# Kernel tuning notes

Hardware: AMD Instinct MI355X
Metric: run time of the kernel (lower is better)

The kernel has to match this reference:

```python
import jax, jax.numpy as jnp
import numpy as np

NUM_ITERATIONS = 5
EPSILON_0 = 1.0
EPS = 1e-20


def setup_inputs() -> dict:
    key = jax.random.key(0)
    k1, k2 = jax.random.split(key)
    B, NIN, NOUT = 8192, 3072, 512
    x = jax.random.uniform(k1, (B, NIN), dtype=jnp.float32)
    w = jax.random.uniform(k2, (NOUT, NIN), dtype=jnp.float32)
    # weights setter normalizes rows to sum to 1
    w = w / w.sum(axis=1, keepdims=True)
    h_initial = jnp.full((NOUT,), 1.0 / NOUT, dtype=jnp.float32)
    return {"x": x, "weights": w, "h_initial": h_initial}


def reference(x, weights, h_initial):
    # x: [B, NIN], weights: [NOUT, NIN], h_initial: [NOUT]
    x = x / (x.sum(axis=1, keepdims=True) + EPS)  # input normalization in forward()
    B = x.shape[0]
    h = jnp.broadcast_to(h_initial[None, :], (B, h_initial.shape[0]))

    def step(h, _):
        # Original: h_w = h[:,:,None]*W[None]; h_w /= h_w.sum(1,keepdim)+eps;
        #           h_w = (h_w * x[:,None,:]).sum(-1)
        # Equivalent without materializing [B, NOUT, NIN]:
        denom = h @ weights                       # [B, NIN] = sum_n h_bn W_nk
        h_w = h * ((x / (denom + EPS)) @ weights.T)  # [B, NOUT]
        h_new = h + EPSILON_0 * h_w               # epsilon_0 > 0 branch
        h_new = h_new / (h_new.sum(axis=1, keepdims=True) + EPS)
        return h_new, None

    h, _ = jax.lax.scan(step, h, None, length=NUM_ITERATIONS)
    return h
```

## Files before the change

kernel.cpp:

```cpp
#include <hip/hip_runtime.h>


#define NIN 3072
#define NOUT 512

using f32x4 = __attribute__((ext_vector_type(4))) float;
using i32x8 = __attribute__((ext_vector_type(8))) int;

union frag32 { i32x8 v; uint4 q[2]; };

#define MFMA128(A, B, C) \
    __builtin_amdgcn_mfma_scale_f32_16x16x128_f8f6f4( \
        (A), (B), (C), 0, 0, 0, (int)0x7f7f7f7f, 0, (int)0x7f7f7f7f)
#define MFMA128_F6(A, B, C) \
    __builtin_amdgcn_mfma_scale_f32_16x16x128_f8f6f4( \
        (A), (B), (C), 0, 2, 0, (int)0x7f7f7f7f, 0, (int)0x7f7f7f7f)

__device__ __forceinline__ unsigned short f2bf(float f) {
    unsigned int u = __builtin_bit_cast(unsigned int, f);
    return (unsigned short)((u + 0x7fffu + ((u >> 16) & 1u)) >> 16);
}
__device__ __forceinline__ float bf2f(unsigned short s) {
    unsigned int u = ((unsigned int)s) << 16;
    return __builtin_bit_cast(float, u);
}

__device__ __forceinline__ unsigned enc_fp6(float p) {
    if (p < 1.9375f) {
        int q = (int)rintf(p * 8.0f);
        return (unsigned)q;
    }
    if (p < 3.875f) {
        int m = (int)rintf((p - 2.0f) * 4.0f);
        return (m > 7) ? 24u : (16u + (unsigned)m);
    }
    int m = (int)rintf((p - 4.0f) * 2.0f);
    if (m > 7) m = 7;
    return 24u + (unsigned)m;
}

__device__ __forceinline__ void load6(frag32& f, const unsigned char* p) {
    const uint2* q = reinterpret_cast<const uint2*>(p);
    uint2 a = q[0], b = q[1], c = q[2];
    f.v = (i32x8){(int)a.x, (int)a.y, (int)b.x, (int)b.y, (int)c.x, (int)c.y, 0, 0};
}

#define LDS_BARRIER() do {                                   \
    asm volatile("s_waitcnt lgkmcnt(0)" ::: "memory");       \
    __builtin_amdgcn_s_barrier();                            \
    asm volatile("" ::: "memory");                           \
} while (0)

__global__ void prep_all(const float* __restrict__ x,
                         const float* __restrict__ W,
                         const float* __restrict__ h_init,
                         unsigned short* __restrict__ X2,
                         unsigned char* __restrict__ W1,
                         unsigned char* __restrict__ W2,
                         float* __restrict__ d0part) {
    __shared__ float tile[64][132];
    __shared__ float wsum[4];
    const int bb = blockIdx.x;
    const int t  = threadIdx.x;

    if (bb < 192) {
        const int s  = bb >> 3, nc = bb & 7;
        const int n0 = nc * 64, k0 = s * 128;

        {
            int r8 = t >> 5, c4 = (t & 31) << 2;
            #pragma unroll
            for (int pass = 0; pass < 8; ++pass) {
                int r = pass * 8 + r8;
                float4 v = *reinterpret_cast<const float4*>(
                    &W[(size_t)(n0 + r) * NIN + k0 + c4]);
                tile[r][c4] = v.x; tile[r][c4 + 1] = v.y;
                tile[r][c4 + 2] = v.z; tile[r][c4 + 3] = v.w;
            }
        }
        __syncthreads();

        {
            int ntl = t >> 6, l = t & 63, lo = l & 15, hi = l >> 4;
            int n_loc = ntl * 16 + lo;
            int kk = hi * 32;
            unsigned int words[8];
            #pragma unroll
            for (int q = 0; q < 8; ++q) {
                float v0 = tile[n_loc][kk + q * 4 + 0] * 4096.0f;
                float v1 = tile[n_loc][kk + q * 4 + 1] * 4096.0f;
                float v2 = tile[n_loc][kk + q * 4 + 2] * 4096.0f;
                float v3 = tile[n_loc][kk + q * 4 + 3] * 4096.0f;
                int pk = __builtin_amdgcn_cvt_pk_fp8_f32(v0, v1, 0, false);
                pk     = __builtin_amdgcn_cvt_pk_fp8_f32(v2, v3, pk, true);
                words[q] = (unsigned int)pk;
            }
            uint4* dst = reinterpret_cast<uint4*>(
                W2 + ((size_t)((s * 32 + nc * 4 + ntl) * 64 + l)) * 32);
            dst[0] = *reinterpret_cast<uint4*>(&words[0]);
            dst[1] = *reinterpret_cast<uint4*>(&words[4]);
        }

        {
            int w8 = t >> 5, r5 = t & 31, l15 = r5 & 15, hs = r5 >> 4;
            int hi = ((nc & 1) << 1) + hs;
            int l  = hi * 16 + l15;
            int c  = nc >> 1;
            int kout_loc = w8 * 16 + l15;
            unsigned int dw[6] = {0, 0, 0, 0, 0, 0};
            #pragma unroll
            for (int j = 0; j < 32; ++j) {
                float p = tile[hs * 32 + j][kout_loc] * 8192.0f;
                unsigned c6 = enc_fp6(p);
                int bit = 6 * j, di = bit >> 5, off = bit & 31;
                dw[di] |= c6 << off;
                if (off > 26) dw[di + 1] |= c6 >> (32 - off);
            }
            uint2* d2 = reinterpret_cast<uint2*>(
                W1 + ((size_t)(((s * 8 + w8) * 4 + c) * 64 + l)) * 24);
            d2[0] = make_uint2(dw[0], dw[1]);
            d2[1] = make_uint2(dw[2], dw[3]);
            d2[2] = make_uint2(dw[4], dw[5]);
        }

        if (t < 128) {
            float ssum = 0.f;
            #pragma unroll 8
            for (int r = 0; r < 64; ++r)
                ssum += h_init[n0 + r] * tile[r][t];
            d0part[(size_t)nc * NIN + k0 + t] = ssum;
        }
    } else {
        const int b = bb - 192;
        const float4* r4 = reinterpret_cast<const float4*>(x + (size_t)b * NIN);
        float s = 0.f;
        float4 v0 = r4[t], v1 = r4[t + 256], v2 = r4[t + 512];
        s = v0.x + v0.y + v0.z + v0.w + v1.x + v1.y + v1.z + v1.w + v2.x + v2.y + v2.z + v2.w;
        #pragma unroll
        for (int off = 32; off > 0; off >>= 1) s += __shfl_down(s, off, 64);
        int w = t >> 6, l = t & 63;
        if (l == 0) wsum[w] = s;
        __syncthreads();
        float inv = 16.0f / (wsum[0] + wsum[1] + wsum[2] + wsum[3] + 1e-20f);
        unsigned short* orow = X2 + (size_t)b * NIN;
        #pragma unroll
        for (int c = 0; c < 3; ++c) {
            float4 v = (c == 0) ? v0 : (c == 1) ? v1 : v2;
            ushort4 o;
            o.x = f2bf(v.x * inv); o.y = f2bf(v.y * inv);
            o.z = f2bf(v.z * inv); o.w = f2bf(v.w * inv);
            *reinterpret_cast<ushort4*>(orow + (t + c * 256) * 4) = o;
        }
    }
}

__global__ __launch_bounds__(512, 1) void nnmf_main(
    const unsigned short* __restrict__ X2,
    const unsigned char* __restrict__ W1,
    const unsigned char* __restrict__ W2,
    const float* __restrict__ d0part,
    const float* __restrict__ h_init,
    float* __restrict__ out)
{
    __shared__ unsigned char  h8_lds[32 * 528];
    __shared__ float          h32_lds[32 * 516];
    __shared__ unsigned short x_lds[32 * 136];
    __shared__ unsigned char  r8_lds[32 * 144];
    __shared__ float red[8][32];

    const int tid = threadIdx.x;
    const int w  = tid >> 6;
    const int l  = tid & 63;
    const int lo = l & 15;
    const int hi = l >> 4;
    const int b0 = blockIdx.x * 32;

    for (int idx = tid; idx < 32 * 512; idx += 512) {
        int r = idx >> 9, c = idx & 511;
        h32_lds[r * 516 + c] = h_init[c];
    }

    const int xrow = tid >> 4, xcc = tid & 15;
    const uint4* xg = reinterpret_cast<const uint4*>(X2 + (size_t)(b0 + xrow) * NIN + xcc * 8);
    unsigned short* xdst = &x_lds[xrow * 136 + xcc * 8];

    const unsigned char* w1base = W1 + ((size_t)(w * 4) * 64 + l) * 24;
    const unsigned char* w2base = W2 + (size_t)w * 8192 + (size_t)l * 32;

    *reinterpret_cast<uint4*>(xdst) = xg[0];
    uint4 xnext = xg[16];
    frag32 w1buf[4];
    __syncthreads();

    const float DSCL = 4.76837158203125e-07f;
    const float TS   = 1.0f / 65536.0f;
    f32x4 tacc[2][4];

    for (int it = 0; it < 5; ++it) {
        #pragma unroll
        for (int m = 0; m < 2; ++m)
            #pragma unroll
            for (int nt = 0; nt < 4; ++nt)
                tacc[m][nt] = (f32x4){0.f, 0.f, 0.f, 0.f};

        for (int s = 0; s < 24; ++s) {
            const int sn  = (s + 1 == 24) ? 0 : s + 1;
            const int sn2 = (s + 2 >= 24) ? (s + 2 - 24) : s + 2;

            frag32 w2v[4];
            {
                const unsigned char* w2p = w2base + (size_t)s * 65536;
                #pragma unroll
                for (int nt = 0; nt < 4; ++nt) {
                    const uint4* p = reinterpret_cast<const uint4*>(w2p + nt * 2048);
                    w2v[nt].q[0] = p[0];
                    w2v[nt].q[1] = p[1];
                }
            }

            f32x4 d0 = {0,0,0,0}, d1 = {0,0,0,0};
            float dv = 0.f;
            if (it == 0) {
                const float* dp = d0part + s * 128 + w * 16 + lo;
                float sm = 1e-20f;
                #pragma unroll
                for (int j = 0; j < 8; ++j) sm += dp[(size_t)j * NIN];
                dv = 1.0f / sm;
            } else {
                #pragma unroll
                for (int c = 0; c < 4; ++c) {
                    frag32 ha0, ha1;
                    const uint4* p0 = reinterpret_cast<const uint4*>(
                        &h8_lds[lo * 528 + c * 128 + hi * 32]);
                    const uint4* p1 = reinterpret_cast<const uint4*>(
                        &h8_lds[(16 + lo) * 528 + c * 128 + hi * 32]);
                    ha0.q[0] = p0[0]; ha0.q[1] = p0[1];
                    ha1.q[0] = p1[0]; ha1.q[1] = p1[1];
                    d0 = MFMA128_F6(ha0.v, w1buf[c].v, d0);
                    d1 = MFMA128_F6(ha1.v, w1buf[c].v, d1);
                }
            }

            #pragma unroll
            for (int i = 0; i < 4; ++i) {
                int row0 = hi * 4 + i;
                float x0 = bf2f(x_lds[row0 * 136 + w * 16 + lo]);
                float x1 = bf2f(x_lds[(16 + row0) * 136 + w * 16 + lo]);
                float r0, r1;
                if (it == 0) { r0 = x0 * dv; r1 = x1 * dv; }
                else {
                    r0 = x0 * __builtin_amdgcn_rcpf(fmaf(d0[i], DSCL, 1e-20f));
                    r1 = x1 * __builtin_amdgcn_rcpf(fmaf(d1[i], DSCL, 1e-20f));
                }
                int c0 = __builtin_amdgcn_cvt_pk_fp8_f32(r0, r0, 0, false);
                int c1 = __builtin_amdgcn_cvt_pk_fp8_f32(r1, r1, 0, false);
                r8_lds[row0 * 144 + w * 16 + lo] = (unsigned char)(c0 & 0xff);
                r8_lds[(16 + row0) * 144 + w * 16 + lo] = (unsigned char)(c1 & 0xff);
            }
            LDS_BARRIER();

            frag32 ra0, ra1;
            {
                const uint4* p0 = reinterpret_cast<const uint4*>(&r8_lds[lo * 144 + hi * 32]);
                const uint4* p1 = reinterpret_cast<const uint4*>(&r8_lds[(16 + lo) * 144 + hi * 32]);
                ra0.q[0] = p0[0]; ra0.q[1] = p0[1];
                ra1.q[0] = p1[0]; ra1.q[1] = p1[1];
            }
            #pragma unroll
            for (int nt = 0; nt < 2; ++nt) {
                tacc[0][nt] = MFMA128(ra0.v, w2v[nt].v, tacc[0][nt]);
                tacc[1][nt] = MFMA128(ra1.v, w2v[nt].v, tacc[1][nt]);
            }

            if (it > 0 || s == 23) {
                const unsigned char* w1p = w1base + (size_t)sn * 49152;
                #pragma unroll
                for (int c = 0; c < 4; ++c)
                    load6(w1buf[c], w1p + c * 1536);
            }

            #pragma unroll
            for (int nt = 2; nt < 4; ++nt) {
                tacc[0][nt] = MFMA128(ra0.v, w2v[nt].v, tacc[0][nt]);
                tacc[1][nt] = MFMA128(ra1.v, w2v[nt].v, tacc[1][nt]);
            }

            *reinterpret_cast<uint4*>(xdst) = xnext;
            xnext = xg[(size_t)sn2 * 16];
            LDS_BARRIER();
        }

        float hv_[2][4][4];
        float p[2][4];
        #pragma unroll
        for (int m = 0; m < 2; ++m)
            #pragma unroll
            for (int i = 0; i < 4; ++i) p[m][i] = 0.f;

        #pragma unroll
        for (int m = 0; m < 2; ++m)
            #pragma unroll
            for (int nt = 0; nt < 4; ++nt)
                #pragma unroll
                for (int i = 0; i < 4; ++i) {
                    int row = m * 16 + hi * 4 + i;
                    int col = w * 64 + nt * 16 + lo;
                    float hv = h32_lds[row * 516 + col];
                    float v = hv * (1.f + tacc[m][nt][i] * TS);
                    hv_[m][nt][i] = v;
                    p[m][i] += v;
                }
        #pragma unroll
        for (int mask = 1; mask < 16; mask <<= 1)
            #pragma unroll
            for (int m = 0; m < 2; ++m)
                #pragma unroll
                for (int i = 0; i < 4; ++i)
                    p[m][i] += __shfl_xor(p[m][i], mask, 64);
        if (lo == 0) {
            #pragma unroll
            for (int m = 0; m < 2; ++m)
                #pragma unroll
                for (int i = 0; i < 4; ++i)
                    red[w][m * 16 + hi * 4 + i] = p[m][i];
        }
        __syncthreads();
        float inv[2][4];
        #pragma unroll
        for (int m = 0; m < 2; ++m)
            #pragma unroll
            for (int i = 0; i < 4; ++i) {
                int row = m * 16 + hi * 4 + i;
                float S = 0.f;
                #pragma unroll
                for (int ww = 0; ww < 8; ++ww) S += red[ww][row];
                inv[m][i] = 1.f / (S + 1e-20f);
            }

        if (it < 4) {
            #pragma unroll
            for (int m = 0; m < 2; ++m)
                #pragma unroll
                for (int nt = 0; nt < 4; ++nt)
                    #pragma unroll
                    for (int i = 0; i < 4; ++i) {
                        int row = m * 16 + hi * 4 + i;
                        int col = w * 64 + nt * 16 + lo;
                        float hv = hv_[m][nt][i] * inv[m][i];
                        h32_lds[row * 516 + col] = hv;
                        int c = __builtin_amdgcn_cvt_pk_fp8_f32(hv * 256.0f, hv * 256.0f, 0, false);
                        h8_lds[row * 528 + col] = (unsigned char)(c & 0xff);
                    }
            __syncthreads();
        } else {
            #pragma unroll
            for (int m = 0; m < 2; ++m)
                #pragma unroll
                for (int nt = 0; nt < 4; ++nt)
                    #pragma unroll
                    for (int i = 0; i < 4; ++i) {
                        int row = m * 16 + hi * 4 + i;
                        int col = w * 64 + nt * 16 + lo;
                        out[(size_t)(b0 + row) * 512 + col] = hv_[m][nt][i] * inv[m][i];
                    }
        }
    }
}

extern "C" void kernel_launch(void* const* d_in, const int* in_sizes, int n_in,
                              void* d_out, int out_size, void* d_ws, size_t ws_size,
                              hipStream_t stream) {
    const float* x   = (const float*)d_in[0];
    const float* wgt = (const float*)d_in[1];
    const float* h0  = (const float*)d_in[2];
    float* out = (float*)d_out;

    unsigned short* X2 = (unsigned short*)d_ws;
    unsigned char*  W1 = (unsigned char*)((char*)d_ws + 50331648);
    unsigned char*  W2 = (unsigned char*)((char*)d_ws + 51511296);
    float* d0part      = (float*)((char*)d_ws + 53084160);

    prep_all<<<8384, 256, 0, stream>>>(x, wgt, h0, X2, W1, W2, d0part);
    nnmf_main<<<256, 512, 0, stream>>>(X2, W1, W2, d0part, h0, out);
}
```

Before: 388.0 us.

## Fuse input row normalization into main kernel, read raw fp32 x directly

Drops the separate pass that normalized x and wrote a bf16 copy to workspace. The main kernel now streams raw fp32 x, accumulates row sums during the first iteration, and folds the normalization factor into the h update. This removes one full read and write of the large input. The cost is twice the x bytes loaded per iteration and a larger LDS tile. The d0part layout is also transposed so it can be read with vector loads.

```diff
diff --git a/kernel.cpp b/kernel.cpp
--- a/kernel.cpp
+++ b/kernel.cpp
@@ -16,15 +16,6 @@
     __builtin_amdgcn_mfma_scale_f32_16x16x128_f8f6f4( \
         (A), (B), (C), 0, 2, 0, (int)0x7f7f7f7f, 0, (int)0x7f7f7f7f)
 
-__device__ __forceinline__ unsigned short f2bf(float f) {
-    unsigned int u = __builtin_bit_cast(unsigned int, f);
-    return (unsigned short)((u + 0x7fffu + ((u >> 16) & 1u)) >> 16);
-}
-__device__ __forceinline__ float bf2f(unsigned short s) {
-    unsigned int u = ((unsigned int)s) << 16;
-    return __builtin_bit_cast(float, u);
-}
-
 __device__ __forceinline__ unsigned enc_fp6(float p) {
     if (p < 1.9375f) {
         int q = (int)rintf(p * 8.0f);
@@ -51,111 +42,84 @@
     asm volatile("" ::: "memory");                           \
 } while (0)
 
-__global__ void prep_all(const float* __restrict__ x,
-                         const float* __restrict__ W,
-                         const float* __restrict__ h_init,
-                         unsigned short* __restrict__ X2,
-                         unsigned char* __restrict__ W1,
-                         unsigned char* __restrict__ W2,
-                         float* __restrict__ d0part) {
+__global__ void prep_w(const float* __restrict__ W,
+                       const float* __restrict__ h_init,
+                       unsigned char* __restrict__ W1,
+                       unsigned char* __restrict__ W2,
+                       float* __restrict__ d0part) {
     __shared__ float tile[64][132];
-    __shared__ float wsum[4];
     const int bb = blockIdx.x;
     const int t  = threadIdx.x;
-
-    if (bb < 192) {
-        const int s  = bb >> 3, nc = bb & 7;
-        const int n0 = nc * 64, k0 = s * 128;
-
-        {
-            int r8 = t >> 5, c4 = (t & 31) << 2;
-            #pragma unroll
-            for (int pass = 0; pass < 8; ++pass) {
-                int r = pass * 8 + r8;
-                float4 v = *reinterpret_cast<const float4*>(
-                    &W[(size_t)(n0 + r) * NIN + k0 + c4]);
-                tile[r][c4] = v.x; tile[r][c4 + 1] = v.y;
-                tile[r][c4 + 2] = v.z; tile[r][c4 + 3] = v.w;
-            }
-        }
-        __syncthreads();
-
-        {
-            int ntl = t >> 6, l = t & 63, lo = l & 15, hi = l >> 4;
-            int n_loc = ntl * 16 + lo;
-            int kk = hi * 32;
-            unsigned int words[8];
-            #pragma unroll
-            for (int q = 0; q < 8; ++q) {
-                float v0 = tile[n_loc][kk + q * 4 + 0] * 4096.0f;
-                float v1 = tile[n_loc][kk + q * 4 + 1] * 4096.0f;
-                float v2 = tile[n_loc][kk + q * 4 + 2] * 4096.0f;
-                float v3 = tile[n_loc][kk + q * 4 + 3] * 4096.0f;
-                int pk = __builtin_amdgcn_cvt_pk_fp8_f32(v0, v1, 0, false);
-                pk     = __builtin_amdgcn_cvt_pk_fp8_f32(v2, v3, pk, true);
-                words[q] = (unsigned int)pk;
-            }
-            uint4* dst = reinterpret_cast<uint4*>(
-                W2 + ((size_t)((s * 32 + nc * 4 + ntl) * 64 + l)) * 32);
-            dst[0] = *reinterpret_cast<uint4*>(&words[0]);
-            dst[1] = *reinterpret_cast<uint4*>(&words[4]);
-        }
-
-        {
-            int w8 = t >> 5, r5 = t & 31, l15 = r5 & 15, hs = r5 >> 4;
-            int hi = ((nc & 1) << 1) + hs;
-            int l  = hi * 16 + l15;
-            int c  = nc >> 1;
-            int kout_loc = w8 * 16 + l15;
-            unsigned int dw[6] = {0, 0, 0, 0, 0, 0};
-            #pragma unroll
-            for (int j = 0; j < 32; ++j) {
-                float p = tile[hs * 32 + j][kout_loc] * 8192.0f;
-                unsigned c6 = enc_fp6(p);
-                int bit = 6 * j, di = bit >> 5, off = bit & 31;
-                dw[di] |= c6 << off;
-                if (off > 26) dw[di + 1] |= c6 >> (32 - off);
-            }
-            uint2* d2 = reinterpret_cast<uint2*>(
-                W1 + ((size_t)(((s * 8 + w8) * 4 + c) * 64 + l)) * 24);
-            d2[0] = make_uint2(dw[0], dw[1]);
-            d2[1] = make_uint2(dw[2], dw[3]);
-            d2[2] = make_uint2(dw[4], dw[5]);
-        }
-
-        if (t < 128) {
-            float ssum = 0.f;
-            #pragma unroll 8
-            for (int r = 0; r < 64; ++r)
-                ssum += h_init[n0 + r] * tile[r][t];
-            d0part[(size_t)nc * NIN + k0 + t] = ssum;
-        }
-    } else {
-        const int b = bb - 192;
-        const float4* r4 = reinterpret_cast<const float4*>(x + (size_t)b * NIN);
-        float s = 0.f;
-        float4 v0 = r4[t], v1 = r4[t + 256], v2 = r4[t + 512];
-        s = v0.x + v0.y + v0.z + v0.w + v1.x + v1.y + v1.z + v1.w + v2.x + v2.y + v2.z + v2.w;
-        #pragma unroll
-        for (int off = 32; off > 0; off >>= 1) s += __shfl_down(s, off, 64);
-        int w = t >> 6, l = t & 63;
-        if (l == 0) wsum[w] = s;
-        __syncthreads();
-        float inv = 16.0f / (wsum[0] + wsum[1] + wsum[2] + wsum[3] + 1e-20f);
-        unsigned short* orow = X2 + (size_t)b * NIN;
-        #pragma unroll
-        for (int c = 0; c < 3; ++c) {
-            float4 v = (c == 0) ? v0 : (c == 1) ? v1 : v2;
-            ushort4 o;
-            o.x = f2bf(v.x * inv); o.y = f2bf(v.y * inv);
-            o.z = f2bf(v.z * inv); o.w = f2bf(v.w * inv);
-            *reinterpret_cast<ushort4*>(orow + (t + c * 256) * 4) = o;
-        }
+    const int s  = bb >> 3, nc = bb & 7;
+    const int n0 = nc * 64, k0 = s * 128;
+
+    {
+        int r8 = t >> 5, c4 = (t & 31) << 2;
+        #pragma unroll
+        for (int pass = 0; pass < 8; ++pass) {
+            int r = pass * 8 + r8;
+            float4 v = *reinterpret_cast<const float4*>(
+                &W[(size_t)(n0 + r) * NIN + k0 + c4]);
+            tile[r][c4] = v.x; tile[r][c4 + 1] = v.y;
+            tile[r][c4 + 2] = v.z; tile[r][c4 + 3] = v.w;
+        }
+    }
+    __syncthreads();
+
+    {
+        int ntl = t >> 6, l = t & 63, lo = l & 15, hi = l >> 4;
+        int n_loc = ntl * 16 + lo;
+        int kk = hi * 32;
+        unsigned int words[8];
+        #pragma unroll
+        for (int q = 0; q < 8; ++q) {
+            float v0 = tile[n_loc][kk + q * 4 + 0] * 4096.0f;
+            float v1 = tile[n_loc][kk + q * 4 + 1] * 4096.0f;
+            float v2 = tile[n_loc][kk + q * 4 + 2] * 4096.0f;
+            float v3 = tile[n_loc][kk + q * 4 + 3] * 4096.0f;
+            int pk = __builtin_amdgcn_cvt_pk_fp8_f32(v0, v1, 0, false);
+            pk     = __builtin_amdgcn_cvt_pk_fp8_f32(v2, v3, pk, true);
+            words[q] = (unsigned int)pk;
+        }
+        uint4* dst = reinterpret_cast<uint4*>(
+            W2 + ((size_t)((s * 32 + nc * 4 + ntl) * 64 + l)) * 32);
+        dst[0] = *reinterpret_cast<uint4*>(&words[0]);
+        dst[1] = *reinterpret_cast<uint4*>(&words[4]);
+    }
+
+    {
+        int w8 = t >> 5, r5 = t & 31, l15 = r5 & 15, hs = r5 >> 4;
+        int hi = ((nc & 1) << 1) + hs;
+        int l  = hi * 16 + l15;
+        int c  = nc >> 1;
+        int kout_loc = w8 * 16 + l15;
+        unsigned int dw[6] = {0, 0, 0, 0, 0, 0};
+        #pragma unroll
+        for (int j = 0; j < 32; ++j) {
+            float p = tile[hs * 32 + j][kout_loc] * 8192.0f;
+            unsigned c6 = enc_fp6(p);
+            int bit = 6 * j, di = bit >> 5, off = bit & 31;
+            dw[di] |= c6 << off;
+            if (off > 26) dw[di + 1] |= c6 >> (32 - off);
+        }
+        uint2* d2 = reinterpret_cast<uint2*>(
+            W1 + ((size_t)(((s * 8 + w8) * 4 + c) * 64 + l)) * 24);
+        d2[0] = make_uint2(dw[0], dw[1]);
+        d2[1] = make_uint2(dw[2], dw[3]);
+        d2[2] = make_uint2(dw[4], dw[5]);
+    }
+
+    if (t < 128) {
+        float ssum = 0.f;
+        #pragma unroll 8
+        for (int r = 0; r < 64; ++r)
+            ssum += h_init[n0 + r] * tile[r][t];
+        d0part[(size_t)(k0 + t) * 8 + nc] = ssum;
     }
 }
 
 __global__ __launch_bounds__(512, 1) void nnmf_main(
-    const unsigned short* __restrict__ X2,
+    const float* __restrict__ x,
     const unsigned char* __restrict__ W1,
     const unsigned char* __restrict__ W2,
     const float* __restrict__ d0part,
@@ -164,9 +128,10 @@
 {
     __shared__ unsigned char  h8_lds[32 * 528];
     __shared__ float          h32_lds[32 * 516];
-    __shared__ unsigned short x_lds[32 * 136];
+    __shared__ float          x_lds[32 * 132];
     __shared__ unsigned char  r8_lds[32 * 144];
     __shared__ float red[8][32];
+    __shared__ float rfac_lds[32];
 
     const int tid = threadIdx.x;
     const int w  = tid >> 6;
@@ -181,20 +146,24 @@
     }
 
     const int xrow = tid >> 4, xcc = tid & 15;
-    const uint4* xg = reinterpret_cast<const uint4*>(X2 + (size_t)(b0 + xrow) * NIN + xcc * 8);
-    unsigned short* xdst = &x_lds[xrow * 136 + xcc * 8];
+    const uint4* xg = reinterpret_cast<const uint4*>(x + (size_t)(b0 + xrow) * NIN);
+    float* xdstA = &x_lds[xrow * 132 + xcc * 4];
+    float* xdstB = &x_lds[xrow * 132 + 64 + xcc * 4];
 
     const unsigned char* w1base = W1 + ((size_t)(w * 4) * 64 + l) * 24;
     const unsigned char* w2base = W2 + (size_t)w * 8192 + (size_t)l * 32;
 
-    *reinterpret_cast<uint4*>(xdst) = xg[0];
-    uint4 xnext = xg[16];
+    *reinterpret_cast<uint4*>(xdstA) = xg[xcc];
+    *reinterpret_cast<uint4*>(xdstB) = xg[16 + xcc];
+    uint4 xnA = xg[32 + xcc], xnB = xg[48 + xcc];
     frag32 w1buf[4];
     __syncthreads();
 
-    const float DSCL = 4.76837158203125e-07f;
-    const float TS   = 1.0f / 65536.0f;
+    const float DSCL2 = 3.0517578125e-05f;
     f32x4 tacc[2][4];
+    float xs0[4], xs1[4];
+    #pragma unroll
+    for (int i = 0; i < 4; ++i) { xs0[i] = 0.f; xs1[i] = 0.f; }
 
     for (int it = 0; it < 5; ++it) {
         #pragma unroll
@@ -221,11 +190,11 @@
             f32x4 d0 = {0,0,0,0}, d1 = {0,0,0,0};
             float dv = 0.f;
             if (it == 0) {
-                const float* dp = d0part + s * 128 + w * 16 + lo;
-                float sm = 1e-20f;
-                #pragma unroll
-                for (int j = 0; j < 8; ++j) sm += dp[(size_t)j * NIN];
-                dv = 1.0f / sm;
+                const float4* dp4 = reinterpret_cast<const float4*>(
+                    d0part + (size_t)(s * 128 + w * 16 + lo) * 8);
+                float4 a = dp4[0], b = dp4[1];
+                float sm = 1e-20f + a.x + a.y + a.z + a.w + b.x + b.y + b.z + b.w;
+                dv = 0.015625f / sm;
             } else {
                 #pragma unroll
                 for (int c = 0; c < 4; ++c) {
@@ -244,13 +213,15 @@
             #pragma unroll
             for (int i = 0; i < 4; ++i) {
                 int row0 = hi * 4 + i;
-                float x0 = bf2f(x_lds[row0 * 136 + w * 16 + lo]);
-                float x1 = bf2f(x_lds[(16 + row0) * 136 + w * 16 + lo]);
+                float x0 = x_lds[row0 * 132 + w * 16 + lo];
+                float x1 = x_lds[(16 + row0) * 132 + w * 16 + lo];
                 float r0, r1;
-                if (it == 0) { r0 = x0 * dv; r1 = x1 * dv; }
-                else {
-                    r0 = x0 * __builtin_amdgcn_rcpf(fmaf(d0[i], DSCL, 1e-20f));
-                    r1 = x1 * __builtin_amdgcn_rcpf(fmaf(d1[i], DSCL, 1e-20f));
+                if (it == 0) {
+                    r0 = x0 * dv; r1 = x1 * dv;
+                    xs0[i] += x0; xs1[i] += x1;
+                } else {
+                    r0 = x0 * __builtin_amdgcn_rcpf(fmaf(d0[i], DSCL2, 1e-20f));
+                    r1 = x1 * __builtin_amdgcn_rcpf(fmaf(d1[i], DSCL2, 1e-20f));
                 }
                 int c0 = __builtin_amdgcn_cvt_pk_fp8_f32(r0, r0, 0, false);
                 int c1 = __builtin_amdgcn_cvt_pk_fp8_f32(r1, r1, 0, false);
@@ -285,17 +256,48 @@
                 tacc[1][nt] = MFMA128(ra1.v, w2v[nt].v, tacc[1][nt]);
             }
 
-            *reinterpret_cast<uint4*>(xdst) = xnext;
-            xnext = xg[(size_t)sn2 * 16];
+            *reinterpret_cast<uint4*>(xdstA) = xnA;
+            *reinterpret_cast<uint4*>(xdstB) = xnB;
+            xnA = xg[(size_t)sn2 * 32 + xcc];
+            xnB = xg[(size_t)sn2 * 32 + 16 + xcc];
             LDS_BARRIER();
+        }
+
+        if (it == 0) {
+            #pragma unroll
+            for (int mask = 1; mask < 16; mask <<= 1)
+                #pragma unroll
+                for (int i = 0; i < 4; ++i) {
+                    xs0[i] += __shfl_xor(xs0[i], mask, 64);
+                    xs1[i] += __shfl_xor(xs1[i], mask, 64);
+                }
+            if (lo == 0) {
+                #pragma unroll
+                for (int i = 0; i < 4; ++i) {
+                    red[w][hi * 4 + i]      = xs0[i];
+                    red[w][16 + hi * 4 + i] = xs1[i];
+                }
+            }
+            __syncthreads();
+            if (tid < 32) {
+                float sme = 1e-20f;
+                #pragma unroll
+                for (int ww = 0; ww < 8; ++ww) sme += red[ww][tid];
+                rfac_lds[tid] = 0.015625f / sme;
+            }
+            __syncthreads();
         }
 
         float hv_[2][4][4];
         float p[2][4];
+        float rf[2][4];
         #pragma unroll
         for (int m = 0; m < 2; ++m)
             #pragma unroll
-            for (int i = 0; i < 4; ++i) p[m][i] = 0.f;
+            for (int i = 0; i < 4; ++i) {
+                p[m][i] = 0.f;
+                rf[m][i] = rfac_lds[m * 16 + hi * 4 + i];
+            }
 
         #pragma unroll
         for (int m = 0; m < 2; ++m)
@@ -306,7 +308,7 @@
                     int row = m * 16 + hi * 4 + i;
                     int col = w * 64 + nt * 16 + lo;
                     float hv = h32_lds[row * 516 + col];
-                    float v = hv * (1.f + tacc[m][nt][i] * TS);
+                    float v = hv * fmaf(tacc[m][nt][i], rf[m][i], 1.0f);
                     hv_[m][nt][i] = v;
                     p[m][i] += v;
                 }
@@ -375,11 +377,10 @@
     const float* h0  = (const float*)d_in[2];
     float* out = (float*)d_out;
 
-    unsigned short* X2 = (unsigned short*)d_ws;
-    unsigned char*  W1 = (unsigned char*)((char*)d_ws + 50331648);
-    unsigned char*  W2 = (unsigned char*)((char*)d_ws + 51511296);
-    float* d0part      = (float*)((char*)d_ws + 53084160);
-
-    prep_all<<<8384, 256, 0, stream>>>(x, wgt, h0, X2, W1, W2, d0part);
-    nnmf_main<<<256, 512, 0, stream>>>(X2, W1, W2, d0part, h0, out);
-}
+    unsigned char* W1 = (unsigned char*)d_ws;
+    unsigned char* W2 = (unsigned char*)((char*)d_ws + 1179648);
+    float* d0part     = (float*)((char*)d_ws + 2752512);
+
+    prep_w<<<192, 256, 0, stream>>>(wgt, h0, W1, W2, d0part);
+    nnmf_main<<<256, 512, 0, stream>>>(x, W1, W2, d0part, h0, out);
+}
```

New measurement: 407.0 us. 4.9% more time.
